# Performance work log

Hardware: AMD Instinct MI355X
Metric: run time of the kernel (lower is better)

The kernel has to match this reference:

```python
import jax, jax.numpy as jnp
import numpy as np


def setup_inputs() -> dict:
    key = jax.random.key(0)
    ks = jax.random.split(key, 5)
    B, M, R = 32, 32, 128
    d_lang, d_region, d_rank, d_fusion = 1024, 2048, 256, 256
    u = jax.random.normal(ks[0], (B, M, d_lang), dtype=jnp.float32)
    v = jax.random.normal(ks[1], (B, R, d_region), dtype=jnp.float32)
    # Linear weights stored torch-style as (out_features, in_features)
    Wu = jax.random.normal(ks[2], (d_rank, d_lang), dtype=jnp.float32) * (1.0 / np.sqrt(d_lang))
    Wv = jax.random.normal(ks[3], (d_rank, d_region), dtype=jnp.float32) * (1.0 / np.sqrt(d_region))
    Wp = jax.random.normal(ks[4], (d_fusion, d_rank), dtype=jnp.float32) * (1.0 / np.sqrt(d_rank))
    bp = jnp.zeros((d_fusion,), dtype=jnp.float32)
    return {"u": u, "v": v, "Wu": Wu, "Wv": Wv, "Wp": Wp, "bp": bp}


def reference(u, v, Wu, Wv, Wp, bp):
    # u: (B, M, d_lang), v: (B, R, d_region)
    up = jnp.einsum('bmd,rd->bmr', u, Wu)          # (B, M, d_rank)  [rd: out x in]
    vp = jnp.einsum('bnd,rd->bnr', v, Wv)          # (B, R, d_rank)
    # broadcast bilinear multiply: (B, M, R, d_rank)
    prod = up[:, :, None, :] * vp[:, None, :, :]
    o = jnp.einsum('bmnk,fk->bmnf', prod, Wp) + bp  # p-linear -> (B, M, R, d_fusion)
    # dropout is identity in inference mode
    return jax.nn.relu(o)
```

## Files before the change

kernel.cpp:

```cpp
#include <hip/hip_runtime.h>
#include <hip/hip_bf16.h>


typedef __attribute__((ext_vector_type(8))) short short8;
typedef __attribute__((ext_vector_type(4))) float floatx4;
typedef __attribute__((ext_vector_type(4))) unsigned uintx4;

__device__ __forceinline__ short f2bf(float f) {
    union { float f; unsigned u; } cv; cv.f = f;
    unsigned r = cv.u + 0x7fffu + ((cv.u >> 16) & 1u);
    return (short)(r >> 16);
}
__device__ __forceinline__ float bf2f(short s) {
    union { unsigned u; float f; } cv;
    cv.u = ((unsigned)(unsigned short)s) << 16; return cv.f;
}
__device__ __forceinline__ unsigned scale2(short a, short b, float ua, float ub) {
    float x = __uint_as_float(((unsigned)(unsigned short)a) << 16) * ua;
    float y = __uint_as_float(((unsigned)(unsigned short)b) << 16) * ub;
    return __builtin_amdgcn_perm(__float_as_uint(y), __float_as_uint(x), 0x07060302);
}

#define GL2LDS(gptr, lptr) __builtin_amdgcn_global_load_lds(                    \
    (const __attribute__((address_space(1))) void*)(gptr),                      \
    (__attribute__((address_space(3))) void*)(lptr), 16, 0, 0)

#define N_U  1048576
#define N_V  8388608
#define N_WU 262144
#define N_WV 524288
#define N_WP 65536

__global__ __launch_bounds__(256) void convert_kernel(
    const float* __restrict__ u, const float* __restrict__ v,
    const float* __restrict__ Wu, const float* __restrict__ Wv,
    const float* __restrict__ Wp, short* __restrict__ dst)
{
    const int n_u = N_U / 4, n_v = N_V / 4, n_wu = N_WU / 4, n_wv = N_WV / 4,
              n_wp = N_WP / 4;
    const int total = n_u + n_v + n_wu + n_wv + n_wp;
    for (int i4 = blockIdx.x * blockDim.x + threadIdx.x; i4 < total;
         i4 += gridDim.x * blockDim.x) {
        const float* src; int off = i4;
        if (off < n_u) src = u;
        else { off -= n_u;
            if (off < n_v) src = v;
            else { off -= n_v;
                if (off < n_wu) src = Wu;
                else { off -= n_wu;
                    if (off < n_wv) src = Wv;
                    else { off -= n_wv; src = Wp; } } } }
        float4 f = *((const float4*)src + off);
        short4 o;
        o.x = f2bf(f.x); o.y = f2bf(f.y); o.z = f2bf(f.z); o.w = f2bf(f.w);
        *((short4*)dst + i4) = o;
    }
}

__global__ __launch_bounds__(256) void proj_kernel(
    const short* __restrict__ Xu, const short* __restrict__ Wgu,
    short* __restrict__ Cu,
    const short* __restrict__ Xv, const short* __restrict__ Wgv,
    short* __restrict__ Cv)
{
    __shared__ short Xs[64 * 32];
    __shared__ short Wsh[64 * 32];

    const int tid  = threadIdx.x;
    const int lane = tid & 63;
    const int wave = tid >> 6;
    const int quad = lane >> 4;
    const int l15  = lane & 15;

    int blk = blockIdx.x;
    const short *X, *W; short* C; int D;
    if (blk < 64) { X = Xu; W = Wgu; C = Cu; D = 1024; }
    else          { blk -= 64; X = Xv; W = Wgv; C = Cv; D = 2048; }
    const int r0 = (blk >> 2) * 64;
    const int c0 = (blk & 3) * 64;
    const int wr = (wave >> 1) * 32;
    const int wc = (wave & 1) * 32;

    const int sr  = tid >> 2;
    const int skg = (tid & 3) * 8;

    floatx4 acc[2][2] = {};

    for (int kc = 0; kc < D; kc += 32) {
        __syncthreads();
        GL2LDS(X + (size_t)(r0 + sr) * D + kc + skg, &Xs[sr * 32 + skg]);
        GL2LDS(W + (size_t)(c0 + sr) * D + kc + skg, &Wsh[sr * 32 + skg]);
        __syncthreads();

        short8 a[2], bfr[2];
#pragma unroll
        for (int t = 0; t < 2; t++)
            a[t] = *(const short8*)&Xs[(wr + t * 16 + l15) * 32 + quad * 8];
#pragma unroll
        for (int t = 0; t < 2; t++)
            bfr[t] = *(const short8*)&Wsh[(wc + t * 16 + l15) * 32 + quad * 8];
#pragma unroll
        for (int tn = 0; tn < 2; tn++)
#pragma unroll
            for (int tf = 0; tf < 2; tf++)
                acc[tn][tf] = __builtin_amdgcn_mfma_f32_16x16x32_bf16(
                    a[tn], bfr[tf], acc[tn][tf], 0, 0, 0);
    }

#pragma unroll
    for (int tn = 0; tn < 2; tn++)
#pragma unroll
        for (int tf = 0; tf < 2; tf++)
#pragma unroll
            for (int r = 0; r < 4; r++) {
                int row = r0 + wr + tn * 16 + quad * 4 + r;
                int col = c0 + wc + tf * 16 + l15;
                C[(size_t)row * 256 + col] = f2bf(acc[tn][tf][r]);
            }
}

__global__ __launch_bounds__(256) void bilinear_kernel(
    const short* __restrict__ up, const short* __restrict__ vp,
    const short* __restrict__ Wp, const float* __restrict__ bp,
    float* __restrict__ out)
{
    __shared__ short vp_s[128 * 32];
    __shared__ short Ws[128 * 32];
    __shared__ float up_s[256];

    const int tid  = threadIdx.x;
    const int lane = tid & 63;
    const int wave = tid >> 6;
    const int quad = lane >> 4;
    const int l15  = lane & 15;

    const int f_blk = blockIdx.x & 1;
    const int bm    = blockIdx.x >> 1;
    const int b     = bm >> 5;
    const int f0    = f_blk * 128;
    const int wn    = (wave >> 1) * 64;
    const int wf    = (wave & 1) * 64;

    up_s[tid] = bf2f(up[(size_t)bm * 256 + tid]);

    const int sr  = tid >> 2;
    const int skg = (tid & 3) * 8;
    const int sn  = tid >> 1;
    const int skh = (tid & 1) * 16;

    floatx4 acc[4][4] = {};

    for (int kc = 0; kc < 256; kc += 32) {
        __syncthreads();
        {
            const short* g = vp + (size_t)(b * 128 + sr) * 256 + kc + skg;
            GL2LDS(g,                 &vp_s[sr * 32 + skg]);
            GL2LDS(g + 64 * 256,      &vp_s[(64 + sr) * 32 + skg]);
        }
        {
            const short* wpp = Wp + (size_t)(f0 + sn) * 256 + kc + skh;
            short8 w0 = *(const short8*)wpp;
            short8 w1 = *(const short8*)(wpp + 8);
            const float* us = &up_s[kc + skh];
            float uv[16];
            *(float4*)&uv[0]  = *(const float4*)(us);
            *(float4*)&uv[4]  = *(const float4*)(us + 4);
            *(float4*)&uv[8]  = *(const float4*)(us + 8);
            *(float4*)&uv[12] = *(const float4*)(us + 12);
            uintx4 o0, o1;
#pragma unroll
            for (int i = 0; i < 4; i++)
                o0[i] = scale2(w0[2 * i], w0[2 * i + 1], uv[2 * i], uv[2 * i + 1]);
#pragma unroll
            for (int i = 0; i < 4; i++)
                o1[i] = scale2(w1[2 * i], w1[2 * i + 1], uv[8 + 2 * i], uv[9 + 2 * i]);
            *(uintx4*)&Ws[sn * 32 + skh]     = o0;
            *(uintx4*)&Ws[sn * 32 + skh + 8] = o1;
        }
        __syncthreads();

        short8 a[4], bfr[4];
#pragma unroll
        for (int t = 0; t < 4; t++)
            a[t] = *(const short8*)&vp_s[(wn + t * 16 + l15) * 32 + quad * 8];
#pragma unroll
        for (int t = 0; t < 4; t++)
            bfr[t] = *(const short8*)&Ws[(wf + t * 16 + l15) * 32 + quad * 8];
#pragma unroll
        for (int tn = 0; tn < 4; tn++)
#pragma unroll
            for (int tf = 0; tf < 4; tf++)
                acc[tn][tf] = __builtin_amdgcn_mfma_f32_16x16x32_bf16(
                    a[tn], bfr[tf], acc[tn][tf], 0, 0, 0);
    }

    float bpv[4];
#pragma unroll
    for (int tf = 0; tf < 4; tf++) bpv[tf] = bp[f0 + wf + tf * 16 + l15];

    const size_t out_base = (size_t)bm * 128 * 256;
#pragma unroll
    for (int tn = 0; tn < 4; tn++)
#pragma unroll
        for (int r = 0; r < 4; r++) {
            int n = wn + tn * 16 + quad * 4 + r;
            float* op = out + out_base + (size_t)n * 256 + f0 + wf + l15;
#pragma unroll
            for (int tf = 0; tf < 4; tf++) {
                float val = acc[tn][tf][r] + bpv[tf];
                op[tf * 16] = fmaxf(val, 0.0f);
            }
        }
}

extern "C" void kernel_launch(void* const* d_in, const int* in_sizes, int n_in,
                              void* d_out, int out_size, void* d_ws, size_t ws_size,
                              hipStream_t stream) {
    const float* u  = (const float*)d_in[0];
    const float* v  = (const float*)d_in[1];
    const float* Wu = (const float*)d_in[2];
    const float* Wv = (const float*)d_in[3];
    const float* Wp = (const float*)d_in[4];
    const float* bp = (const float*)d_in[5];
    float* out = (float*)d_out;

    short* bf    = (short*)d_ws;
    short* u_bf  = bf;
    short* v_bf  = u_bf + N_U;
    short* Wu_bf = v_bf + N_V;
    short* Wv_bf = Wu_bf + N_WU;
    short* Wp_bf = Wv_bf + N_WV;
    short* up_bf = Wp_bf + N_WP;
    short* vp_bf = up_bf + 262144;

    convert_kernel<<<dim3(2048), dim3(256), 0, stream>>>(u, v, Wu, Wv, Wp, bf);
    proj_kernel<<<dim3(320), dim3(256), 0, stream>>>(
        u_bf, Wu_bf, up_bf, v_bf, Wv_bf, vp_bf);
    bilinear_kernel<<<dim3(2048), dim3(256), 0, stream>>>(
        up_bf, vp_bf, Wp_bf, bp, out);
}
```

Baseline: 214.3 us.

## Read fp32 Wp directly, widen K step, swap MFMA operands for vectorized stores

The bilinear kernel now reads Wp in fp32 straight from global memory, scales it by up, and truncates to bf16 in registers. This removes Wp from the conversion pass. The K loop steps by 64 with two LDS stages and a padded Ws stride, which halves the number of barriers. Swapping the MFMA operand order makes each lane hold four consecutive output columns, so both the proj and bilinear epilogues write packed bf16 pairs and float4 rows instead of scalars, and the convert kernel uses packed RNE conversion. In exchange, truncation replaces rounding on the scaled weights, and each block reads fp32 Wp, twice the bytes of the old bf16 copy.

```diff
diff --git a/kernel.cpp b/kernel.cpp
--- a/kernel.cpp
+++ b/kernel.cpp
@@ -15,10 +15,13 @@
     union { unsigned u; float f; } cv;
     cv.u = ((unsigned)(unsigned short)s) << 16; return cv.f;
 }
-__device__ __forceinline__ unsigned scale2(short a, short b, float ua, float ub) {
-    float x = __uint_as_float(((unsigned)(unsigned short)a) << 16) * ua;
-    float y = __uint_as_float(((unsigned)(unsigned short)b) << 16) * ub;
-    return __builtin_amdgcn_perm(__float_as_uint(y), __float_as_uint(x), 0x07060302);
+__device__ __forceinline__ unsigned trunc2(float a, float b) {
+    return __builtin_amdgcn_perm(__float_as_uint(b), __float_as_uint(a), 0x07060302);
+}
+__device__ __forceinline__ unsigned rne2(float a, float b) {
+    unsigned ua = __float_as_uint(a); ua += 0x7fffu + ((ua >> 16) & 1u);
+    unsigned ub = __float_as_uint(b); ub += 0x7fffu + ((ub >> 16) & 1u);
+    return __builtin_amdgcn_perm(ub, ua, 0x07060302);
 }
 
 #define GL2LDS(gptr, lptr) __builtin_amdgcn_global_load_lds(                    \
@@ -29,16 +32,14 @@
 #define N_V  8388608
 #define N_WU 262144
 #define N_WV 524288
-#define N_WP 65536
 
 __global__ __launch_bounds__(256) void convert_kernel(
     const float* __restrict__ u, const float* __restrict__ v,
     const float* __restrict__ Wu, const float* __restrict__ Wv,
-    const float* __restrict__ Wp, short* __restrict__ dst)
+    short* __restrict__ dst)
 {
-    const int n_u = N_U / 4, n_v = N_V / 4, n_wu = N_WU / 4, n_wv = N_WV / 4,
-              n_wp = N_WP / 4;
-    const int total = n_u + n_v + n_wu + n_wv + n_wp;
+    const int n_u = N_U / 4, n_v = N_V / 4, n_wu = N_WU / 4, n_wv = N_WV / 4;
+    const int total = n_u + n_v + n_wu + n_wv;
     for (int i4 = blockIdx.x * blockDim.x + threadIdx.x; i4 < total;
          i4 += gridDim.x * blockDim.x) {
         const float* src; int off = i4;
@@ -47,13 +48,12 @@
             if (off < n_v) src = v;
             else { off -= n_v;
                 if (off < n_wu) src = Wu;
-                else { off -= n_wu;
-                    if (off < n_wv) src = Wv;
-                    else { off -= n_wv; src = Wp; } } } }
+                else { off -= n_wu; src = Wv; } } }
         float4 f = *((const float4*)src + off);
-        short4 o;
-        o.x = f2bf(f.x); o.y = f2bf(f.y); o.z = f2bf(f.z); o.w = f2bf(f.w);
-        *((short4*)dst + i4) = o;
+        uint2 o;
+        o.x = rne2(f.x, f.y);
+        o.y = rne2(f.z, f.w);
+        *((uint2*)dst + i4) = o;
     }
 }
 
@@ -104,28 +104,29 @@
 #pragma unroll
             for (int tf = 0; tf < 2; tf++)
                 acc[tn][tf] = __builtin_amdgcn_mfma_f32_16x16x32_bf16(
-                    a[tn], bfr[tf], acc[tn][tf], 0, 0, 0);
+                    bfr[tf], a[tn], acc[tn][tf], 0, 0, 0);
     }
 
 #pragma unroll
     for (int tn = 0; tn < 2; tn++)
 #pragma unroll
-        for (int tf = 0; tf < 2; tf++)
-#pragma unroll
-            for (int r = 0; r < 4; r++) {
-                int row = r0 + wr + tn * 16 + quad * 4 + r;
-                int col = c0 + wc + tf * 16 + l15;
-                C[(size_t)row * 256 + col] = f2bf(acc[tn][tf][r]);
-            }
+        for (int tf = 0; tf < 2; tf++) {
+            int xrow  = r0 + wr + tn * 16 + l15;
+            int cbase = c0 + wc + tf * 16 + quad * 4;
+            uint2 pk;
+            pk.x = rne2(acc[tn][tf][0], acc[tn][tf][1]);
+            pk.y = rne2(acc[tn][tf][2], acc[tn][tf][3]);
+            *(uint2*)&C[(size_t)xrow * 256 + cbase] = pk;
+        }
 }
 
 __global__ __launch_bounds__(256) void bilinear_kernel(
     const short* __restrict__ up, const short* __restrict__ vp,
-    const short* __restrict__ Wp, const float* __restrict__ bp,
+    const float* __restrict__ Wp, const float* __restrict__ bp,
     float* __restrict__ out)
 {
-    __shared__ short vp_s[128 * 32];
-    __shared__ short Ws[128 * 32];
+    __shared__ short vp_s[2][128 * 32];
+    __shared__ short Ws[128 * 72];
     __shared__ float up_s[256];
 
     const int tid  = threadIdx.x;
@@ -143,74 +144,80 @@
 
     up_s[tid] = bf2f(up[(size_t)bm * 256 + tid]);
 
-    const int sr  = tid >> 2;
-    const int skg = (tid & 3) * 8;
-    const int sn  = tid >> 1;
-    const int skh = (tid & 1) * 16;
+    const int sr   = tid >> 2;
+    const int skg  = (tid & 3) * 8;
+    const int wrow = tid >> 1;
+    const int kh   = (tid & 1) * 32;
 
     floatx4 acc[4][4] = {};
 
-    for (int kc = 0; kc < 256; kc += 32) {
+    for (int kc = 0; kc < 256; kc += 64) {
         __syncthreads();
         {
             const short* g = vp + (size_t)(b * 128 + sr) * 256 + kc + skg;
-            GL2LDS(g,                 &vp_s[sr * 32 + skg]);
-            GL2LDS(g + 64 * 256,      &vp_s[(64 + sr) * 32 + skg]);
+            GL2LDS(g,                 &vp_s[0][sr * 32 + skg]);
+            GL2LDS(g + 64 * 256,      &vp_s[0][(64 + sr) * 32 + skg]);
+            GL2LDS(g + 32,            &vp_s[1][sr * 32 + skg]);
+            GL2LDS(g + 64 * 256 + 32, &vp_s[1][(64 + sr) * 32 + skg]);
         }
         {
-            const short* wpp = Wp + (size_t)(f0 + sn) * 256 + kc + skh;
-            short8 w0 = *(const short8*)wpp;
-            short8 w1 = *(const short8*)(wpp + 8);
-            const float* us = &up_s[kc + skh];
-            float uv[16];
-            *(float4*)&uv[0]  = *(const float4*)(us);
-            *(float4*)&uv[4]  = *(const float4*)(us + 4);
-            *(float4*)&uv[8]  = *(const float4*)(us + 8);
-            *(float4*)&uv[12] = *(const float4*)(us + 12);
-            uintx4 o0, o1;
-#pragma unroll
-            for (int i = 0; i < 4; i++)
-                o0[i] = scale2(w0[2 * i], w0[2 * i + 1], uv[2 * i], uv[2 * i + 1]);
-#pragma unroll
-            for (int i = 0; i < 4; i++)
-                o1[i] = scale2(w1[2 * i], w1[2 * i + 1], uv[8 + 2 * i], uv[9 + 2 * i]);
-            *(uintx4*)&Ws[sn * 32 + skh]     = o0;
-            *(uintx4*)&Ws[sn * 32 + skh + 8] = o1;
-        }
-        __syncthreads();
-
-        short8 a[4], bfr[4];
-#pragma unroll
-        for (int t = 0; t < 4; t++)
-            a[t] = *(const short8*)&vp_s[(wn + t * 16 + l15) * 32 + quad * 8];
-#pragma unroll
-        for (int t = 0; t < 4; t++)
-            bfr[t] = *(const short8*)&Ws[(wf + t * 16 + l15) * 32 + quad * 8];
-#pragma unroll
-        for (int tn = 0; tn < 4; tn++)
-#pragma unroll
-            for (int tf = 0; tf < 4; tf++)
-                acc[tn][tf] = __builtin_amdgcn_mfma_f32_16x16x32_bf16(
-                    a[tn], bfr[tf], acc[tn][tf], 0, 0, 0);
-    }
-
-    float bpv[4];
-#pragma unroll
-    for (int tf = 0; tf < 4; tf++) bpv[tf] = bp[f0 + wf + tf * 16 + l15];
+            const float* wpr = Wp + (size_t)(f0 + wrow) * 256 + kc + kh;
+            const float* usr = &up_s[kc + kh];
+#pragma unroll
+            for (int h = 0; h < 4; h++) {
+                float w[8], uu[8];
+                *(float4*)&w[0]  = *(const float4*)(wpr + 8 * h);
+                *(float4*)&w[4]  = *(const float4*)(wpr + 8 * h + 4);
+                *(float4*)&uu[0] = *(const float4*)(usr + 8 * h);
+                *(float4*)&uu[4] = *(const float4*)(usr + 8 * h + 4);
+                uintx4 o;
+#pragma unroll
+                for (int i = 0; i < 4; i++)
+                    o[i] = trunc2(w[2 * i] * uu[2 * i], w[2 * i + 1] * uu[2 * i + 1]);
+                *(uintx4*)&Ws[wrow * 72 + kh + 8 * h] = o;
+            }
+        }
+        __syncthreads();
+
+#pragma unroll
+        for (int kk2 = 0; kk2 < 2; kk2++) {
+            short8 a[4], bfr[4];
+#pragma unroll
+            for (int t = 0; t < 4; t++)
+                a[t] = *(const short8*)&vp_s[kk2][(wn + t * 16 + l15) * 32 + quad * 8];
+#pragma unroll
+            for (int t = 0; t < 4; t++)
+                bfr[t] = *(const short8*)&Ws[(wf + t * 16 + l15) * 72 + kk2 * 32 + quad * 8];
+#pragma unroll
+            for (int tn = 0; tn < 4; tn++)
+#pragma unroll
+                for (int tf = 0; tf < 4; tf++)
+                    acc[tn][tf] = __builtin_amdgcn_mfma_f32_16x16x32_bf16(
+                        bfr[tf], a[tn], acc[tn][tf], 0, 0, 0);
+        }
+    }
+
+    float4 bpv[4];
+#pragma unroll
+    for (int tf = 0; tf < 4; tf++)
+        bpv[tf] = *(const float4*)&bp[f0 + wf + tf * 16 + quad * 4];
 
     const size_t out_base = (size_t)bm * 128 * 256;
 #pragma unroll
-    for (int tn = 0; tn < 4; tn++)
-#pragma unroll
-        for (int r = 0; r < 4; r++) {
-            int n = wn + tn * 16 + quad * 4 + r;
-            float* op = out + out_base + (size_t)n * 256 + f0 + wf + l15;
-#pragma unroll
-            for (int tf = 0; tf < 4; tf++) {
-                float val = acc[tn][tf][r] + bpv[tf];
-                op[tf * 16] = fmaxf(val, 0.0f);
-            }
-        }
+    for (int tn = 0; tn < 4; tn++) {
+        const int n = wn + tn * 16 + l15;
+        float* orow = out + out_base + (size_t)n * 256;
+#pragma unroll
+        for (int tf = 0; tf < 4; tf++) {
+            const int fbase = f0 + wf + tf * 16 + quad * 4;
+            float4 o;
+            o.x = fmaxf(acc[tn][tf][0] + bpv[tf].x, 0.0f);
+            o.y = fmaxf(acc[tn][tf][1] + bpv[tf].y, 0.0f);
+            o.z = fmaxf(acc[tn][tf][2] + bpv[tf].z, 0.0f);
+            o.w = fmaxf(acc[tn][tf][3] + bpv[tf].w, 0.0f);
+            *(float4*)(orow + fbase) = o;
+        }
+    }
 }
 
 extern "C" void kernel_launch(void* const* d_in, const int* in_sizes, int n_in,
@@ -229,13 +236,12 @@
     short* v_bf  = u_bf + N_U;
     short* Wu_bf = v_bf + N_V;
     short* Wv_bf = Wu_bf + N_WU;
-    short* Wp_bf = Wv_bf + N_WV;
-    short* up_bf = Wp_bf + N_WP;
+    short* up_bf = Wv_bf + N_WV;
     short* vp_bf = up_bf + 262144;
 
-    convert_kernel<<<dim3(2048), dim3(256), 0, stream>>>(u, v, Wu, Wv, Wp, bf);
+    convert_kernel<<<dim3(2048), dim3(256), 0, stream>>>(u, v, Wu, Wv, bf);
     proj_kernel<<<dim3(320), dim3(256), 0, stream>>>(
         u_bf, Wu_bf, up_bf, v_bf, Wv_bf, vp_bf);
     bilinear_kernel<<<dim3(2048), dim3(256), 0, stream>>>(
-        up_bf, vp_bf, Wp_bf, bp, out);
-}
+        up_bf, vp_bf, Wp, bp, out);
+}
```

New measurement: 231.0 us. +7.8%, slower.
